# Kernel tuning notes

Hardware: AMD Instinct MI355X
Metric: run time of the kernel (lower is better)

Reference implementation:

```python
import jax, jax.numpy as jnp
import numpy as np

OUT_F, IN_F = 11008, 4096
GROUP = 64                      # group_size, axis=0 grouping
G = OUT_F * IN_F // GROUP       # number of groups = 704512


def setup_inputs() -> dict:
    key = jax.random.key(0)
    ks = jax.random.split(key, 7)
    x = jax.random.normal(ks[0], (512, IN_F), dtype=jnp.float32)
    # packed 4-bit weights: two nibbles per byte, packed along the group axis
    W_q = jax.random.randint(ks[1], (GROUP // 2, G), 0, 256, dtype=jnp.int32)
    # per-group dequant params (scale = 1/quant_scale in the torch code)
    scale = jax.random.uniform(ks[2], (1, G), dtype=jnp.float32) * 0.01 + 1e-4
    zero = jax.random.uniform(ks[3], (1, G), dtype=jnp.float32) * 15.0
    # low-rank correction (LoRC): W_eff = W_dq + U @ V
    U = jax.random.normal(ks[4], (OUT_F, 32), dtype=jnp.float32) * 0.02
    V = jax.random.normal(ks[5], (32, IN_F), dtype=jnp.float32) * 0.02
    bias = jax.random.normal(ks[6], (OUT_F,), dtype=jnp.float32)
    return {"x": x, "W_q": W_q, "scale": scale, "zero": zero,
            "U": U, "V": V, "bias": bias}


def _dequantize(W_q, scale, zero):
    # unpack_4bit_u8: high nibble -> first half of rows, low nibble -> second half
    hi = ((W_q >> 4) & 0xF).astype(jnp.float32)   # [32, G]
    lo = (W_q & 0xF).astype(jnp.float32)          # [32, G]
    Wg = jnp.concatenate([hi, lo], axis=0)        # [64, G] = [group_size, G]
    W = (Wg - zero) * scale                       # per-group affine dequant
    return W.reshape(OUT_F, IN_F)


def reference(x, W_q, scale, zero, U, V, bias):
    W = _dequantize(W_q, scale, zero)             # [out, in]
    W = W + U @ V                                 # low-rank correction
    # nn.Linear semantics: out = x @ W.T + bias
    return x @ W.T + bias
```

## Files before the change

### kernel.cpp

```cpp
#include <hip/hip_runtime.h>
#include <cstdint>

typedef short  s16x8 __attribute__((ext_vector_type(8)));
typedef float  f32x4 __attribute__((ext_vector_type(4)));
typedef int    i32x4 __attribute__((ext_vector_type(4)));
typedef int    i32x2 __attribute__((ext_vector_type(2)));
typedef unsigned short u16x4 __attribute__((ext_vector_type(4)));

#define OUT_F 11008
#define IN_F  4096
#define MROWS 512
#define GQ4   176128
#define HALF  5504
#define RMOD  172

__device__ __forceinline__ unsigned short f2bf(float f) {
  unsigned u = __builtin_bit_cast(unsigned, f);
  return (unsigned short)((u + 0x8000u) >> 16);
}
__device__ __forceinline__ float bfbits(unsigned bits) {
  return __builtin_bit_cast(float, bits);
}
__device__ __forceinline__ unsigned cvtpk(float a, float b) {
  unsigned r;
  asm("v_cvt_pk_bf16_f32 %0, %1, %2" : "=v"(r) : "v"(a), "v"(b));
  return r;
}

__global__ __launch_bounds__(256) void convert_k(const float* __restrict__ x,
                                                 const float* __restrict__ U,
                                                 const float* __restrict__ scale,
                                                 const float* __restrict__ zero,
                                                 unsigned short* __restrict__ xbf,
                                                 unsigned short* __restrict__ Ubf,
                                                 f32x4* __restrict__ mz) {
  int i = blockIdx.x * 256 + threadIdx.x;
  const int NX = (MROWS * IN_F) / 4;
  const int NU = (OUT_F * 32) / 4;
  const int NS = 704512 / 4;
  if (i < NX + NU) {
    const float* src; unsigned short* dst; int idx;
    if (i < NX) { src = x; dst = xbf; idx = i; }
    else        { src = U; dst = Ubf; idx = i - NX; }
    f32x4 v = *(const f32x4*)(src + (size_t)idx * 4);
    u16x4 o;
    o[0] = f2bf(v[0]); o[1] = f2bf(v[1]); o[2] = f2bf(v[2]); o[3] = f2bf(v[3]);
    *(u16x4*)(dst + (size_t)idx * 4) = o;
  } else {
    int idx = i - NX - NU;
    if (idx >= NS) return;
    f32x4 s = *(const f32x4*)(scale + (size_t)idx * 4);
    f32x4 z = *(const f32x4*)(zero  + (size_t)idx * 4);
    f32x4 m;
#pragma unroll
    for (int e = 0; e < 4; ++e) m[e] = -(z[e] + 128.f) * s[e];
    mz[idx] = m;
  }
}

__global__ __launch_bounds__(256) void pcalc_k(const float* __restrict__ x,
                                               const float* __restrict__ V,
                                               float* __restrict__ P) {
  int m  = (blockIdx.x >> 3) * 8 + (threadIdx.x >> 5);
  int j  = threadIdx.x & 31;
  int k0 = (blockIdx.x & 7) * 512;
  const float* xr = x + (size_t)m * IN_F + k0;
  const float* vr = V + (size_t)j * IN_F + k0;
  float a = 0.f;
#pragma unroll 4
  for (int k = 0; k < 512; k += 4) {
    f32x4 xv = *(const f32x4*)(xr + k);
    f32x4 vv = *(const f32x4*)(vr + k);
    a += xv[0]*vv[0] + xv[1]*vv[1] + xv[2]*vv[2] + xv[3]*vv[3];
  }
  atomicAdd(P + m * 32 + j, a);
}

__global__ __launch_bounds__(256, 3) void milo_gemm(
    const unsigned short* __restrict__ xbf,
    const i32x4*          __restrict__ Wq4,
    const f32x4*          __restrict__ Sc4,
    const f32x4*          __restrict__ Mz4,
    const float*          __restrict__ Pf,
    const i32x4*          __restrict__ Ubf4,
    const float*          __restrict__ bias,
    float*                __restrict__ out)
{
  extern __shared__ __align__(16) unsigned short smem[];

  const int tid  = threadIdx.x;
  const int lane = tid & 63;
  const int wid  = tid >> 6;
  const int wm   = wid >> 1;
  const int wn   = wid & 1;

  const int b  = blockIdx.x;
  const int L  = (b & 7) * 86 + (b >> 3);
  const int gn = L >> 2;
  const int gm = L & 3;
  const int m0 = gm * 128;
  const int o0 = gn * 32;

  unsigned wq_off[2], sc_off[2];
#pragma unroll
  for (int p = 0; p < 2; ++p) {
    int tr = (tid >> 4) + p * 16;
    int o  = o0 + tr;
    int g  = o / RMOD;
    int r  = o - g * RMOD;
    wq_off[p] = (unsigned)g * GQ4 + (unsigned)r * 1024u + (tid & 15);
    sc_off[p] = (unsigned)r * 1024u + (tid & 15);
  }
  unsigned a_src[4];
#pragma unroll
  for (int it = 0; it < 4; ++it) {
    int row   = it * 32 + wid * 8 + (lane >> 3);
    int chunk = (lane & 7) ^ ((lane >> 3) & 7);
    a_src[it] = (unsigned)(m0 + row) * IN_F + chunk * 8;
  }

  const int akey   = (lane & 7) << 3;
  const int a_base = (wm * 64 + (lane & 15)) * 64 + ((lane >> 4) * 8);
  const int b_base = (wn * 32 + (lane & 15)) * 64 + ((lane >> 4) * 8);

  f32x4 acc[4][2];
  {
    f32x4 zf = {0.f, 0.f, 0.f, 0.f};
#pragma unroll
    for (int i = 0; i < 4; ++i)
#pragma unroll
      for (int j = 0; j < 2; ++j) acc[i][j] = zf;
  }

  i32x4 wq[2]; f32x4 s4[2], mz4[2];
  f32x4 pf[4]; i32x4 uuF;

  auto issueA = [&](int buf, int k0s) {
    unsigned short* Adst = smem + buf * 8192;
#pragma unroll
    for (int it = 0; it < 4; ++it) {
      __builtin_amdgcn_global_load_lds(
          (const __attribute__((address_space(1))) unsigned int*)(xbf + a_src[it] + k0s),
          (__attribute__((address_space(3))) unsigned int*)(Adst + (it * 32 + wid * 8) * 64),
          16, 0, 0);
    }
  };
  auto loadB = [&](int kq) {
#pragma unroll
    for (int p = 0; p < 2; ++p) {
      wq[p]  = Wq4[wq_off[p] + kq];
      s4[p]  = Sc4[sc_off[p] + kq];
      mz4[p] = Mz4[sc_off[p] + kq];
    }
  };
  auto writeB = [&](int buf) {
    unsigned short* Bn = smem + 16384 + buf * 4096;
#pragma unroll
    for (int p = 0; p < 2; ++p) {
      int tr   = (tid >> 4) + p * 16;
      int scol = ((tid & 15) * 4) ^ ((tr & 7) << 3);
      float h[4], l[4];
#pragma unroll
      for (int e = 0; e < 4; ++e) {
        int v = wq[p][e];
        float qh = bfbits(0x43000000u | (((unsigned)v & 0xF0u) << 12));
        float ql = bfbits(0x43000000u | (((unsigned)v & 0x0Fu) << 16));
        h[e] = __builtin_fmaf(qh, s4[p][e], mz4[p][e]);
        l[e] = __builtin_fmaf(ql, s4[p][e], mz4[p][e]);
      }
      i32x2 hh = { (int)cvtpk(h[0], h[1]), (int)cvtpk(h[2], h[3]) };
      i32x2 ll = { (int)cvtpk(l[0], l[1]), (int)cvtpk(l[2], l[3]) };
      *(i32x2*)(Bn + tr * 64 + scol)        = hh;
      *(i32x2*)(Bn + (tr + 32) * 64 + scol) = ll;
    }
  };
  auto loadF = [&]() {
    int row = tid >> 1, h = tid & 1;
#pragma unroll
    for (int q = 0; q < 4; ++q)
      pf[q] = *(const f32x4*)(Pf + (m0 + row) * 32 + h * 16 + q * 4);
    int rw = tid >> 2, h4 = tid & 3;
    int oc = (rw < 32) ? (o0 + rw) : (HALF + o0 + rw - 32);
    uuF = Ubf4[oc * 4 + h4];
  };
  auto writeF = [&](int buf) {
    unsigned short* An = smem + buf * 8192;
    unsigned short* Bn = smem + 16384 + buf * 4096;
    i32x4 zi = {0, 0, 0, 0};
    {
      int row = tid >> 1, h = tid & 1;
      int key = (row & 7) << 3;
#pragma unroll
      for (int q = 0; q < 4; ++q) {
        i32x2 t2 = { (int)cvtpk(pf[q][0], pf[q][1]),
                     (int)cvtpk(pf[q][2], pf[q][3]) };
        *(i32x2*)(An + row * 64 + ((h * 16 + q * 4) ^ key)) = t2;
      }
#pragma unroll
      for (int q = 0; q < 2; ++q)
        *(i32x4*)(An + row * 64 + ((32 + h * 16 + q * 8) ^ key)) = zi;
    }
    {
      int rw = tid >> 2, h4 = tid & 3;
      int key = (rw & 7) << 3;
      *(i32x4*)(Bn + rw * 64 + ((h4 * 8) ^ key))      = uuF;
      *(i32x4*)(Bn + rw * 64 + ((32 + h4 * 8) ^ key)) = zi;
    }
  };
  auto compute = [&](int buf) {
    const unsigned short* Ac = smem + buf * 8192;
    const unsigned short* Bc = smem + 16384 + buf * 4096;
#pragma unroll
    for (int kk = 0; kk < 64; kk += 32) {
      s16x8 av[4], bv[2];
#pragma unroll
      for (int f = 0; f < 4; ++f)
        av[f] = *(const s16x8*)(Ac + ((a_base + f * 1024 + kk) ^ akey));
#pragma unroll
      for (int f = 0; f < 2; ++f)
        bv[f] = *(const s16x8*)(Bc + ((b_base + f * 1024 + kk) ^ akey));
#pragma unroll
      for (int i = 0; i < 4; ++i)
#pragma unroll
        for (int j = 0; j < 2; ++j)
          acc[i][j] = __builtin_amdgcn_mfma_f32_16x16x32_bf16(av[i], bv[j], acc[i][j], 0, 0, 0);
    }
  };

  loadB(0);
  issueA(0, 0);
  writeB(0);
  __syncthreads();

  for (int t = 0; t < 63; ++t) {
    int cur = t & 1, nxt = cur ^ 1;
    loadB((t + 1) * 16);
    issueA(nxt, (t + 1) * 64);
    compute(cur);
    writeB(nxt);
    __syncthreads();
  }
  loadF();
  compute(1);
  writeF(0);
  __syncthreads();
  compute(0);

#pragma unroll
  for (int fn = 0; fn < 2; ++fn) {
    int c = wn * 32 + fn * 16 + (lane & 15);
    int o = (c < 32) ? (o0 + c) : (HALF + o0 + (c - 32));
    float bv = bias[o];
#pragma unroll
    for (int fm = 0; fm < 4; ++fm) {
      int m = m0 + wm * 64 + fm * 16 + ((lane >> 4) << 2);
#pragma unroll
      for (int j = 0; j < 4; ++j)
        out[(size_t)(m + j) * OUT_F + o] = acc[fm][fn][j] + bv;
    }
  }
}

extern "C" void kernel_launch(void* const* d_in, const int* in_sizes, int n_in,
                              void* d_out, int out_size, void* d_ws, size_t ws_size,
                              hipStream_t stream) {
  const float* x     = (const float*)d_in[0];
  const int*   Wq    = (const int*)d_in[1];
  const float* scale = (const float*)d_in[2];
  const float* zero  = (const float*)d_in[3];
  const float* U     = (const float*)d_in[4];
  const float* V     = (const float*)d_in[5];
  const float* bias  = (const float*)d_in[6];
  float* out = (float*)d_out;

  unsigned short* xbf = (unsigned short*)d_ws;
  unsigned short* Ubf = xbf + (size_t)MROWS * IN_F;
  float*          P   = (float*)(Ubf + (size_t)OUT_F * 32);
  float*          mz  = P + (size_t)MROWS * 32;

  (void)hipMemsetAsync(P, 0, (size_t)MROWS * 32 * sizeof(float), stream);
  convert_k<<<3080, 256, 0, stream>>>(x, U, scale, zero, xbf, Ubf, (f32x4*)mz);
  pcalc_k<<<512, 256, 0, stream>>>(x, V, P);
  milo_gemm<<<688, 256, 49152, stream>>>(xbf, (const i32x4*)Wq,
                                         (const f32x4*)scale, (const f32x4*)mz,
                                         P, (const i32x4*)Ubf, bias, out);
}
```

Before: 140.8 us.

## Prefetch quantized weights two stages ahead with manual waitcnt barriers and MFMA priority

Double-buffers the packed-weight, scale and zero register loads so global fetches run two K-steps ahead of their dequantize-and-store to LDS. The loop is unrolled by two, and __syncthreads is replaced by explicit lgkmcnt/vmcnt waits plus s_barrier, so the next stage's weight loads can stay in flight across the barrier. It also raises wave priority around the MFMA block. The aim is to hide global-memory latency for B behind compute, at the cost of more registers and hand-managed wait counts that depend on the exact order in which loads are issued.

```diff
diff --git a/kernel.cpp b/kernel.cpp
--- a/kernel.cpp
+++ b/kernel.cpp
@@ -132,7 +132,8 @@
       for (int j = 0; j < 2; ++j) acc[i][j] = zf;
   }
 
-  i32x4 wq[2]; f32x4 s4[2], mz4[2];
+  i32x4 wqS0[2], wqS1[2];
+  f32x4 s4S0[2], mzS0[2], s4S1[2], mzS1[2];
   f32x4 pf[4]; i32x4 uuF;
 
   auto issueA = [&](int buf, int k0s) {
@@ -145,15 +146,16 @@
           16, 0, 0);
     }
   };
-  auto loadB = [&](int kq) {
+  auto loadB = [&](int kq, i32x4 (&wq)[2], f32x4 (&s4)[2], f32x4 (&mz)[2]) {
 #pragma unroll
     for (int p = 0; p < 2; ++p) {
-      wq[p]  = Wq4[wq_off[p] + kq];
-      s4[p]  = Sc4[sc_off[p] + kq];
-      mz4[p] = Mz4[sc_off[p] + kq];
-    }
-  };
-  auto writeB = [&](int buf) {
+      wq[p] = Wq4[wq_off[p] + kq];
+      s4[p] = Sc4[sc_off[p] + kq];
+      mz[p] = Mz4[sc_off[p] + kq];
+    }
+  };
+  auto writeB = [&](int buf, const i32x4 (&wq)[2], const f32x4 (&s4)[2],
+                    const f32x4 (&mz)[2]) {
     unsigned short* Bn = smem + 16384 + buf * 4096;
 #pragma unroll
     for (int p = 0; p < 2; ++p) {
@@ -165,8 +167,8 @@
         int v = wq[p][e];
         float qh = bfbits(0x43000000u | (((unsigned)v & 0xF0u) << 12));
         float ql = bfbits(0x43000000u | (((unsigned)v & 0x0Fu) << 16));
-        h[e] = __builtin_fmaf(qh, s4[p][e], mz4[p][e]);
-        l[e] = __builtin_fmaf(ql, s4[p][e], mz4[p][e]);
+        h[e] = __builtin_fmaf(qh, s4[p][e], mz[p][e]);
+        l[e] = __builtin_fmaf(ql, s4[p][e], mz[p][e]);
       }
       i32x2 hh = { (int)cvtpk(h[0], h[1]), (int)cvtpk(h[2], h[3]) };
       i32x2 ll = { (int)cvtpk(l[0], l[1]), (int)cvtpk(l[2], l[3]) };
@@ -210,6 +212,7 @@
   auto compute = [&](int buf) {
     const unsigned short* Ac = smem + buf * 8192;
     const unsigned short* Bc = smem + 16384 + buf * 4096;
+    __builtin_amdgcn_s_setprio(1);
 #pragma unroll
     for (int kk = 0; kk < 64; kk += 32) {
       s16x8 av[4], bv[2];
@@ -225,25 +228,46 @@
         for (int j = 0; j < 2; ++j)
           acc[i][j] = __builtin_amdgcn_mfma_f32_16x16x32_bf16(av[i], bv[j], acc[i][j], 0, 0, 0);
     }
-  };
-
-  loadB(0);
+    __builtin_amdgcn_s_setprio(0);
+  };
+
+#define WAIT_LGKM0 asm volatile("s_waitcnt lgkmcnt(0)" ::: "memory")
+#define WAIT_VM(N) asm volatile("s_waitcnt vmcnt(" #N ")" ::: "memory")
+
   issueA(0, 0);
-  writeB(0);
-  __syncthreads();
-
-  for (int t = 0; t < 63; ++t) {
-    int cur = t & 1, nxt = cur ^ 1;
-    loadB((t + 1) * 16);
-    issueA(nxt, (t + 1) * 64);
-    compute(cur);
-    writeB(nxt);
-    __syncthreads();
-  }
+  loadB(0,  wqS0, s4S0, mzS0);
+  loadB(16, wqS1, s4S1, mzS1);
+  writeB(0, wqS0, s4S0, mzS0);
+  WAIT_LGKM0;
+  __builtin_amdgcn_s_barrier();
+
+  for (int tt = 0; tt < 62; tt += 2) {
+    issueA(1, (tt + 1) * 64);
+    writeB(1, wqS1, s4S1, mzS1);
+    loadB((tt + 2) * 16, wqS0, s4S0, mzS0);
+    compute(0);
+    WAIT_LGKM0;
+    WAIT_VM(6);
+    __builtin_amdgcn_s_barrier();
+    issueA(0, (tt + 2) * 64);
+    writeB(0, wqS0, s4S0, mzS0);
+    loadB((tt + 3) * 16, wqS1, s4S1, mzS1);
+    compute(1);
+    WAIT_LGKM0;
+    WAIT_VM(6);
+    __builtin_amdgcn_s_barrier();
+  }
+  issueA(1, 63 * 64);
+  writeB(1, wqS1, s4S1, mzS1);
+  compute(0);
+  WAIT_LGKM0;
+  WAIT_VM(0);
+  __builtin_amdgcn_s_barrier();
   loadF();
   compute(1);
   writeF(0);
-  __syncthreads();
+  WAIT_LGKM0;
+  __builtin_amdgcn_s_barrier();
   compute(0);
 
 #pragma unroll
@@ -259,6 +283,8 @@
         out[(size_t)(m + j) * OUT_F + o] = acc[fm][fn][j] + bv;
     }
   }
+#undef WAIT_LGKM0
+#undef WAIT_VM
 }
 
 extern "C" void kernel_launch(void* const* d_in, const int* in_sizes, int n_in,
```

New measurement: 138.6 us. No clear change (-1.5%).

## Split GEMM tile across eight waves and raise MFMA priority

Applied to the files above, without the earlier changes.

The GEMM block grows from 256 to 512 threads while keeping the same 128x64 output tile. Each wave now owns 32 rows instead of 64, and the A/B loads and epilogue stores are redistributed so each thread moves half as much data. The aim is lower per-wave register pressure and more resident waves per CU to hide global-load and dequantisation latency. The compute phase is also wrapped in s_setprio so MFMA issue is favoured over other waves. In exchange, each wave reuses fewer LDS fragments per MFMA, and the barriers now synchronise twice as many waves.

```diff
diff --git a/kernel.cpp b/kernel.cpp
--- a/kernel.cpp
+++ b/kernel.cpp
@@ -76,7 +76,7 @@
   atomicAdd(P + m * 32 + j, a);
 }
 
-__global__ __launch_bounds__(256, 3) void milo_gemm(
+__global__ __launch_bounds__(512, 6) void milo_gemm(
     const unsigned short* __restrict__ xbf,
     const i32x4*          __restrict__ Wq4,
     const f32x4*          __restrict__ Sc4,
@@ -101,130 +101,118 @@
   const int m0 = gm * 128;
   const int o0 = gn * 32;
 
-  unsigned wq_off[2], sc_off[2];
-#pragma unroll
-  for (int p = 0; p < 2; ++p) {
-    int tr = (tid >> 4) + p * 16;
-    int o  = o0 + tr;
-    int g  = o / RMOD;
-    int r  = o - g * RMOD;
-    wq_off[p] = (unsigned)g * GQ4 + (unsigned)r * 1024u + (tid & 15);
-    sc_off[p] = (unsigned)r * 1024u + (tid & 15);
-  }
-  unsigned a_src[4];
-#pragma unroll
-  for (int it = 0; it < 4; ++it) {
-    int row   = it * 32 + wid * 8 + (lane >> 3);
-    int chunk = (lane & 7) ^ ((lane >> 3) & 7);
+  const int tr = tid >> 4;
+  unsigned wq_off, sc_off;
+  {
+    int o = o0 + tr;
+    int g = o / RMOD;
+    int r = o - g * RMOD;
+    wq_off = (unsigned)g * GQ4 + (unsigned)r * 1024u + (tid & 15);
+    sc_off = (unsigned)r * 1024u + (tid & 15);
+  }
+  unsigned a_src[2];
+#pragma unroll
+  for (int it = 0; it < 2; ++it) {
+    int row   = wid * 16 + it * 8 + (lane >> 3);
+    int chunk = (lane & 7) ^ (lane >> 3);
     a_src[it] = (unsigned)(m0 + row) * IN_F + chunk * 8;
   }
 
   const int akey   = (lane & 7) << 3;
-  const int a_base = (wm * 64 + (lane & 15)) * 64 + ((lane >> 4) * 8);
+  const int a_base = (wm * 32 + (lane & 15)) * 64 + ((lane >> 4) * 8);
   const int b_base = (wn * 32 + (lane & 15)) * 64 + ((lane >> 4) * 8);
 
-  f32x4 acc[4][2];
+  f32x4 acc[2][2];
   {
     f32x4 zf = {0.f, 0.f, 0.f, 0.f};
 #pragma unroll
-    for (int i = 0; i < 4; ++i)
+    for (int i = 0; i < 2; ++i)
 #pragma unroll
       for (int j = 0; j < 2; ++j) acc[i][j] = zf;
   }
 
-  i32x4 wq[2]; f32x4 s4[2], mz4[2];
-  f32x4 pf[4]; i32x4 uuF;
+  i32x4 wq; f32x4 s4, mz4;
+  f32x4 pf[2]; i32x4 uuF;
 
   auto issueA = [&](int buf, int k0s) {
     unsigned short* Adst = smem + buf * 8192;
 #pragma unroll
-    for (int it = 0; it < 4; ++it) {
+    for (int it = 0; it < 2; ++it) {
       __builtin_amdgcn_global_load_lds(
           (const __attribute__((address_space(1))) unsigned int*)(xbf + a_src[it] + k0s),
-          (__attribute__((address_space(3))) unsigned int*)(Adst + (it * 32 + wid * 8) * 64),
+          (__attribute__((address_space(3))) unsigned int*)(Adst + (wid * 16 + it * 8) * 64),
           16, 0, 0);
     }
   };
   auto loadB = [&](int kq) {
-#pragma unroll
-    for (int p = 0; p < 2; ++p) {
-      wq[p]  = Wq4[wq_off[p] + kq];
-      s4[p]  = Sc4[sc_off[p] + kq];
-      mz4[p] = Mz4[sc_off[p] + kq];
-    }
+    wq  = Wq4[wq_off + kq];
+    s4  = Sc4[sc_off + kq];
+    mz4 = Mz4[sc_off + kq];
   };
   auto writeB = [&](int buf) {
     unsigned short* Bn = smem + 16384 + buf * 4096;
-#pragma unroll
-    for (int p = 0; p < 2; ++p) {
-      int tr   = (tid >> 4) + p * 16;
-      int scol = ((tid & 15) * 4) ^ ((tr & 7) << 3);
-      float h[4], l[4];
-#pragma unroll
-      for (int e = 0; e < 4; ++e) {
-        int v = wq[p][e];
-        float qh = bfbits(0x43000000u | (((unsigned)v & 0xF0u) << 12));
-        float ql = bfbits(0x43000000u | (((unsigned)v & 0x0Fu) << 16));
-        h[e] = __builtin_fmaf(qh, s4[p][e], mz4[p][e]);
-        l[e] = __builtin_fmaf(ql, s4[p][e], mz4[p][e]);
-      }
-      i32x2 hh = { (int)cvtpk(h[0], h[1]), (int)cvtpk(h[2], h[3]) };
-      i32x2 ll = { (int)cvtpk(l[0], l[1]), (int)cvtpk(l[2], l[3]) };
-      *(i32x2*)(Bn + tr * 64 + scol)        = hh;
-      *(i32x2*)(Bn + (tr + 32) * 64 + scol) = ll;
-    }
+    int scol = ((tid & 15) * 4) ^ ((tr & 7) << 3);
+    float h[4], l[4];
+#pragma unroll
+    for (int e = 0; e < 4; ++e) {
+      int v = wq[e];
+      float qh = bfbits(0x43000000u | (((unsigned)v & 0xF0u) << 12));
+      float ql = bfbits(0x43000000u | (((unsigned)v & 0x0Fu) << 16));
+      h[e] = __builtin_fmaf(qh, s4[e], mz4[e]);
+      l[e] = __builtin_fmaf(ql, s4[e], mz4[e]);
+    }
+    i32x2 hh = { (int)cvtpk(h[0], h[1]), (int)cvtpk(h[2], h[3]) };
+    i32x2 ll = { (int)cvtpk(l[0], l[1]), (int)cvtpk(l[2], l[3]) };
+    *(i32x2*)(Bn + tr * 64 + scol)        = hh;
+    *(i32x2*)(Bn + (tr + 32) * 64 + scol) = ll;
   };
   auto loadF = [&]() {
-    int row = tid >> 1, h = tid & 1;
-#pragma unroll
-    for (int q = 0; q < 4; ++q)
-      pf[q] = *(const f32x4*)(Pf + (m0 + row) * 32 + h * 16 + q * 4);
-    int rw = tid >> 2, h4 = tid & 3;
+    int row = tid >> 2, h4 = tid & 3;
+#pragma unroll
+    for (int q = 0; q < 2; ++q)
+      pf[q] = *(const f32x4*)(Pf + (m0 + row) * 32 + h4 * 8 + q * 4);
+    int rw = tid >> 3, h8 = tid & 7;
     int oc = (rw < 32) ? (o0 + rw) : (HALF + o0 + rw - 32);
-    uuF = Ubf4[oc * 4 + h4];
+    uuF = Ubf4[oc * 4 + (h8 & 3)];
   };
   auto writeF = [&](int buf) {
     unsigned short* An = smem + buf * 8192;
     unsigned short* Bn = smem + 16384 + buf * 4096;
     i32x4 zi = {0, 0, 0, 0};
     {
-      int row = tid >> 1, h = tid & 1;
+      int row = tid >> 2, h4 = tid & 3;
       int key = (row & 7) << 3;
-#pragma unroll
-      for (int q = 0; q < 4; ++q) {
-        i32x2 t2 = { (int)cvtpk(pf[q][0], pf[q][1]),
-                     (int)cvtpk(pf[q][2], pf[q][3]) };
-        *(i32x2*)(An + row * 64 + ((h * 16 + q * 4) ^ key)) = t2;
-      }
-#pragma unroll
-      for (int q = 0; q < 2; ++q)
-        *(i32x4*)(An + row * 64 + ((32 + h * 16 + q * 8) ^ key)) = zi;
+      i32x4 t4 = { (int)cvtpk(pf[0][0], pf[0][1]), (int)cvtpk(pf[0][2], pf[0][3]),
+                   (int)cvtpk(pf[1][0], pf[1][1]), (int)cvtpk(pf[1][2], pf[1][3]) };
+      *(i32x4*)(An + row * 64 + ((h4 * 8) ^ key))      = t4;
+      *(i32x4*)(An + row * 64 + ((32 + h4 * 8) ^ key)) = zi;
     }
     {
-      int rw = tid >> 2, h4 = tid & 3;
+      int rw = tid >> 3, h8 = tid & 7;
       int key = (rw & 7) << 3;
-      *(i32x4*)(Bn + rw * 64 + ((h4 * 8) ^ key))      = uuF;
-      *(i32x4*)(Bn + rw * 64 + ((32 + h4 * 8) ^ key)) = zi;
+      *(i32x4*)(Bn + rw * 64 + ((h8 * 8) ^ key)) = (h8 < 4) ? uuF : zi;
     }
   };
   auto compute = [&](int buf) {
     const unsigned short* Ac = smem + buf * 8192;
     const unsigned short* Bc = smem + 16384 + buf * 4096;
+    __builtin_amdgcn_s_setprio(1);
 #pragma unroll
     for (int kk = 0; kk < 64; kk += 32) {
-      s16x8 av[4], bv[2];
-#pragma unroll
-      for (int f = 0; f < 4; ++f)
+      s16x8 av[2], bv[2];
+#pragma unroll
+      for (int f = 0; f < 2; ++f)
         av[f] = *(const s16x8*)(Ac + ((a_base + f * 1024 + kk) ^ akey));
 #pragma unroll
       for (int f = 0; f < 2; ++f)
         bv[f] = *(const s16x8*)(Bc + ((b_base + f * 1024 + kk) ^ akey));
 #pragma unroll
-      for (int i = 0; i < 4; ++i)
+      for (int i = 0; i < 2; ++i)
 #pragma unroll
         for (int j = 0; j < 2; ++j)
           acc[i][j] = __builtin_amdgcn_mfma_f32_16x16x32_bf16(av[i], bv[j], acc[i][j], 0, 0, 0);
     }
+    __builtin_amdgcn_s_setprio(0);
   };
 
   loadB(0);
@@ -252,8 +240,8 @@
     int o = (c < 32) ? (o0 + c) : (HALF + o0 + (c - 32));
     float bv = bias[o];
 #pragma unroll
-    for (int fm = 0; fm < 4; ++fm) {
-      int m = m0 + wm * 64 + fm * 16 + ((lane >> 4) << 2);
+    for (int fm = 0; fm < 2; ++fm) {
+      int m = m0 + wm * 32 + fm * 16 + ((lane >> 4) << 2);
 #pragma unroll
       for (int j = 0; j < 4; ++j)
         out[(size_t)(m + j) * OUT_F + o] = acc[fm][fn][j] + bv;
@@ -281,7 +269,7 @@
   (void)hipMemsetAsync(P, 0, (size_t)MROWS * 32 * sizeof(float), stream);
   convert_k<<<3080, 256, 0, stream>>>(x, U, scale, zero, xbf, Ubf, (f32x4*)mz);
   pcalc_k<<<512, 256, 0, stream>>>(x, V, P);
-  milo_gemm<<<688, 256, 49152, stream>>>(xbf, (const i32x4*)Wq,
+  milo_gemm<<<688, 512, 49152, stream>>>(xbf, (const i32x4*)Wq,
                                          (const f32x4*)scale, (const f32x4*)mz,
                                          P, (const i32x4*)Ubf, bias, out);
 }
```

New measurement: 142.6 us. Within noise of the previous version (+1.3%).
